# Kernel optimization log

Measured on AMD Instinct MI355X. Metric: run time of the kernel, lower is better.

The kernel has to match this reference:

```python
import jax, jax.numpy as jnp
import numpy as np

NODES, NFEAT = 128, 256


def setup_inputs() -> dict:
    key = jax.random.key(0)
    k1, k2, k3, k4, k5, k6 = jax.random.split(key, 6)
    B = 512
    x = jax.random.normal(k1, (B, NODES, NFEAT), dtype=jnp.float32)
    adj = jax.random.uniform(k2, (B, NODES, NODES), dtype=jnp.float32)
    # GraphConvolution(nfeat, nfeat): weight [nfeat, nfeat], bias [nfeat]
    s = 1.0 / np.sqrt(NFEAT)
    gcn_w = jax.random.uniform(k3, (NFEAT, NFEAT), minval=-s, maxval=s, dtype=jnp.float32)
    gcn_b = jax.random.uniform(k4, (NFEAT,), minval=-s, maxval=s, dtype=jnp.float32)
    # fc: Linear(nfeat*nodes, nfeat), torch layout [out, in]
    s2 = 1.0 / np.sqrt(NFEAT * NODES)
    fc_w = jax.random.uniform(k5, (NFEAT, NFEAT * NODES), minval=-s2, maxval=s2, dtype=jnp.float32)
    fc_b = jax.random.uniform(k6, (NFEAT,), minval=-s2, maxval=s2, dtype=jnp.float32)
    return {"x": x, "adj": adj, "gcn_w": gcn_w, "gcn_b": gcn_b, "fc_w": fc_w, "fc_b": fc_b}


def reference(x, adj, gcn_w, gcn_b, fc_w, fc_b):
    B = x.shape[0]
    # Per-sample loop GCN fused as batched matmuls:
    # support = X @ W ; out = A @ support + b
    support = jnp.einsum('bnf,fg->bng', x, gcn_w)          # [B, nodes, nfeat]
    mid = jnp.einsum('bnm,bmg->bng', adj, support) + gcn_b  # [B, nodes, nfeat]
    # cat along dim0 then reshape(-1, nfeat*nodes) == per-graph flatten
    flat = mid.reshape(B, NODES * NFEAT)
    output = flat @ fc_w.T + fc_b                           # [B, nfeat]
    useful_input = x[:, 0, :]                               # [B, nfeat]
    return (output, useful_input, output)
```

## Files before the change

kernel.cpp:

```cpp
#include <hip/hip_runtime.h>

#define NODES 128
#define NFEAT 256
#define BATCH 512
#define KTOT  (NODES * NFEAT)
#define SPLIT 64
#define KCH   (KTOT / SPLIT)

typedef __bf16 bf16_t;
typedef bf16_t bf16x8 __attribute__((ext_vector_type(8)));
typedef float  f32x4  __attribute__((ext_vector_type(4)));

#define BK   32
#define LDK  40
#define LDM  136
#define TILE 128

__device__ __forceinline__ bf16x8 cvt8(const float4 a, const float4 b) {
    bf16x8 t;
    t[0] = (bf16_t)a.x; t[1] = (bf16_t)a.y; t[2] = (bf16_t)a.z; t[3] = (bf16_t)a.w;
    t[4] = (bf16_t)b.x; t[5] = (bf16_t)b.y; t[6] = (bf16_t)b.z; t[7] = (bf16_t)b.w;
    return t;
}

struct XT { float4 v[4]; };
__device__ __forceinline__ void xload(const float* __restrict__ src, int ld, int k0,
                                      int tid, XT& t) {
#pragma unroll
    for (int i = 0; i < 2; i++) {
        int f = tid + i * 256, r = f >> 2, c = f & 3;
        t.v[2 * i]     = *(const float4*)(src + (size_t)r * ld + k0 + c * 8);
        t.v[2 * i + 1] = *(const float4*)(src + (size_t)r * ld + k0 + c * 8 + 4);
    }
}
__device__ __forceinline__ void xstore(bf16_t* __restrict__ dst, int tid, const XT& t) {
#pragma unroll
    for (int i = 0; i < 2; i++) {
        int f = tid + i * 256, r = f >> 2, c = f & 3;
        *(bf16x8*)(dst + r * LDK + c * 8) = cvt8(t.v[2 * i], t.v[2 * i + 1]);
    }
}

struct AT { bf16x8 v[2]; };
__device__ __forceinline__ void aload(const bf16_t* __restrict__ src, int ld, int k0,
                                      int tid, AT& t) {
#pragma unroll
    for (int i = 0; i < 2; i++) {
        int f = tid + i * 256, r = f >> 2, c = f & 3;
        t.v[i] = *(const bf16x8*)(src + (size_t)r * ld + k0 + c * 8);
    }
}
__device__ __forceinline__ void astore(bf16_t* __restrict__ dst, int tid, const AT& t) {
#pragma unroll
    for (int i = 0; i < 2; i++) {
        int f = tid + i * 256, r = f >> 2, c = f & 3;
        *(bf16x8*)(dst + r * LDK + c * 8) = t.v[i];
    }
}

__global__ __launch_bounds__(256)
void k_wt(const float* __restrict__ w, bf16_t* __restrict__ wT) {
    const int g0 = blockIdx.x * 4;
    const int k  = threadIdx.x;
    const float4 v = *(const float4*)(w + (size_t)k * NFEAT + g0);
    wT[(size_t)(g0 + 0) * NFEAT + k] = (bf16_t)v.x;
    wT[(size_t)(g0 + 1) * NFEAT + k] = (bf16_t)v.y;
    wT[(size_t)(g0 + 2) * NFEAT + k] = (bf16_t)v.z;
    wT[(size_t)(g0 + 3) * NFEAT + k] = (bf16_t)v.w;
}

__global__ __launch_bounds__(256, 3)
void k_fused12(const float* __restrict__ x, const float* __restrict__ adj,
               const bf16_t* __restrict__ wT, const float* __restrict__ gcn_b,
               bf16_t* __restrict__ mid) {
    __shared__ __align__(16) bf16_t As[TILE * LDK];
    __shared__ __align__(16) bf16_t Sb[TILE * LDM];
    const int n0  = blockIdx.x * TILE;
    const int b   = blockIdx.y;
    const int tid = threadIdx.x;
    const int lane = tid & 63, w = tid >> 6, wm = w & 1, wn = w >> 1;
    const int l15 = lane & 15, q = lane >> 4;
    const float* xb   = x   + (size_t)b * NODES * NFEAT;
    const float* adjb = adj + (size_t)b * NODES * NODES;

    const bf16_t* wrow[4];
#pragma unroll
    for (int j = 0; j < 4; j++)
        wrow[j] = wT + (size_t)(n0 + wn * 64 + j * 16 + l15) * NFEAT + q * 8;

    f32x4 acc[4][4] = {};
    {
        XT xt; xload(xb, NFEAT, 0, tid, xt);
        bf16x8 bcur[4], bnxt[4];
#pragma unroll
        for (int j = 0; j < 4; j++) bcur[j] = *(const bf16x8*)(wrow[j]);
        xstore(As, tid, xt);
        __syncthreads();
        for (int k0 = 0; k0 < NFEAT; k0 += BK) {
            const int kn = k0 + BK;
            const bool in = kn < NFEAT;
            XT xn;
            if (in) xload(xb, NFEAT, kn, tid, xn);
            const int knc = in ? kn : 0;
#pragma unroll
            for (int j = 0; j < 4; j++) bnxt[j] = *(const bf16x8*)(wrow[j] + knc);
            bf16x8 a[4];
#pragma unroll
            for (int i = 0; i < 4; i++)
                a[i] = *(const bf16x8*)(As + (wm * 64 + i * 16 + l15) * LDK + q * 8);
#pragma unroll
            for (int i = 0; i < 4; i++)
#pragma unroll
                for (int j = 0; j < 4; j++)
                    acc[i][j] = __builtin_amdgcn_mfma_f32_16x16x32_bf16(a[i], bcur[j], acc[i][j], 0, 0, 0);
            __syncthreads();
            if (in) xstore(As, tid, xn);
#pragma unroll
            for (int j = 0; j < 4; j++) bcur[j] = bnxt[j];
            __syncthreads();
        }
    }

    XT at; xload(adjb, NODES, 0, tid, at);
#pragma unroll
    for (int i = 0; i < 4; i++)
#pragma unroll
        for (int j = 0; j < 4; j++)
#pragma unroll
            for (int r = 0; r < 4; r++) {
                int m = wm * 64 + i * 16 + q * 4 + r;
                int g = wn * 64 + j * 16 + l15;
                Sb[g * LDM + m] = (bf16_t)acc[i][j][r];
            }
    __syncthreads();
    xstore(As, tid, at);
    __syncthreads();

    f32x4 acc2[4][4] = {};
    for (int k0 = 0; k0 < NODES; k0 += BK) {
        const int kn = k0 + BK;
        const bool in = kn < NODES;
        XT xn;
        if (in) xload(adjb, NODES, kn, tid, xn);
        bf16x8 a[4], bb[4];
#pragma unroll
        for (int i = 0; i < 4; i++)
            a[i] = *(const bf16x8*)(As + (wm * 64 + i * 16 + l15) * LDK + q * 8);
#pragma unroll
        for (int j = 0; j < 4; j++)
            bb[j] = *(const bf16x8*)(Sb + (wn * 64 + j * 16 + l15) * LDM + k0 + q * 8);
#pragma unroll
        for (int i = 0; i < 4; i++)
#pragma unroll
            for (int j = 0; j < 4; j++)
                acc2[i][j] = __builtin_amdgcn_mfma_f32_16x16x32_bf16(a[i], bb[j], acc2[i][j], 0, 0, 0);
        __syncthreads();
        if (in) xstore(As, tid, xn);
        __syncthreads();
    }
    bf16_t* outb = mid + (size_t)b * NODES * NFEAT;
#pragma unroll
    for (int j = 0; j < 4; j++) {
        int g = n0 + wn * 64 + j * 16 + l15;
        float bias = gcn_b[g];
#pragma unroll
        for (int i = 0; i < 4; i++)
#pragma unroll
            for (int r = 0; r < 4; r++) {
                int node = wm * 64 + i * 16 + q * 4 + r;
                outb[(size_t)node * NFEAT + g] = (bf16_t)(acc2[i][j][r] + bias);
            }
    }
}

__global__ __launch_bounds__(256, 2)
void k_out(const bf16_t* __restrict__ flat, const float* __restrict__ fcw,
           bf16_t* __restrict__ part) {
    __shared__ __align__(16) bf16_t As[TILE * LDK];
    __shared__ __align__(16) bf16_t Bs[TILE * LDK];
    const int m0 = blockIdx.x * TILE;
    const int n0 = blockIdx.y * TILE;
    const int kb = blockIdx.z * KCH, kend = kb + KCH;
    const int tid = threadIdx.x;
    const int lane = tid & 63, w = tid >> 6, wm = w & 1, wn = w >> 1;
    const int l15 = lane & 15, q = lane >> 4;
    f32x4 acc[4][4] = {};
    const bf16_t* fa = flat + (size_t)m0 * KTOT;
    const float*  fb = fcw + (size_t)n0 * KTOT;

    AT a0; aload(fa, KTOT, kb, tid, a0);
    XT b0; xload(fb, KTOT, kb, tid, b0);
    astore(As, tid, a0);
    xstore(Bs, tid, b0);
    __syncthreads();
    for (int k0 = kb; k0 < kend; k0 += BK) {
        const int kn = k0 + BK;
        const bool in = kn < kend;
        AT an; XT bn;
        if (in) { aload(fa, KTOT, kn, tid, an); xload(fb, KTOT, kn, tid, bn); }
        bf16x8 a[4], bbf[4];
#pragma unroll
        for (int i = 0; i < 4; i++)
            a[i] = *(const bf16x8*)(As + (wm * 64 + i * 16 + l15) * LDK + q * 8);
#pragma unroll
        for (int j = 0; j < 4; j++)
            bbf[j] = *(const bf16x8*)(Bs + (wn * 64 + j * 16 + l15) * LDK + q * 8);
#pragma unroll
        for (int i = 0; i < 4; i++)
#pragma unroll
            for (int j = 0; j < 4; j++)
                acc[i][j] = __builtin_amdgcn_mfma_f32_16x16x32_bf16(a[i], bbf[j], acc[i][j], 0, 0, 0);
        __syncthreads();
        if (in) { astore(As, tid, an); xstore(Bs, tid, bn); }
        __syncthreads();
    }
    bf16_t* pb = part + (size_t)blockIdx.z * BATCH * NFEAT;
#pragma unroll
    for (int i = 0; i < 4; i++)
#pragma unroll
        for (int j = 0; j < 4; j++)
#pragma unroll
            for (int r = 0; r < 4; r++) {
                int bt = m0 + wm * 64 + i * 16 + q * 4 + r;
                int o  = n0 + wn * 64 + j * 16 + l15;
                pb[(size_t)bt * NFEAT + o] = (bf16_t)acc[i][j][r];
            }
}

__global__ __launch_bounds__(256)
void k_reduce(const bf16_t* __restrict__ part, const float* __restrict__ fc_b,
              const float* __restrict__ x, float* __restrict__ out) {
    const int g = blockIdx.x * 256 + threadIdx.x;
    const int o = g & (NFEAT - 1), b = g >> 8;
    float s = fc_b[o];
#pragma unroll
    for (int i = 0; i < SPLIT; i++)
        s += (float)part[(size_t)i * BATCH * NFEAT + g];
    out[g] = s;
    out[BATCH * NFEAT + g] = x[(size_t)b * NODES * NFEAT + o];
    out[2 * BATCH * NFEAT + g] = s;
}

extern "C" void kernel_launch(void* const* d_in, const int* in_sizes, int n_in,
                              void* d_out, int out_size, void* d_ws, size_t ws_size,
                              hipStream_t stream) {
    const float* x     = (const float*)d_in[0];
    const float* adj   = (const float*)d_in[1];
    const float* gcn_w = (const float*)d_in[2];
    const float* gcn_b = (const float*)d_in[3];
    const float* fc_w  = (const float*)d_in[4];
    const float* fc_b  = (const float*)d_in[5];
    float* out = (float*)d_out;

    bf16_t* wT   = (bf16_t*)d_ws;
    bf16_t* mid  = (bf16_t*)((char*)d_ws + 131072);
    bf16_t* part = (bf16_t*)((char*)d_ws + 131072 + (size_t)BATCH * NODES * NFEAT * 2);

    k_wt     <<<dim3(64), dim3(256), 0, stream>>>(gcn_w, wT);
    k_fused12<<<dim3(2, BATCH), dim3(256), 0, stream>>>(x, adj, wT, gcn_b, mid);
    k_out    <<<dim3(4, 2, SPLIT), dim3(256), 0, stream>>>(mid, fc_w, part);
    k_reduce <<<dim3(BATCH), dim3(256), 0, stream>>>(part, fc_b, x, out);
}
```

Before: 209.7 us.

## Replace split-K partial buffer with atomic accumulation, deepen prefetch, widen K tile

New measurement: 238.9 us. 13.9% more time.

```diff
diff --git a/kernel.cpp b/kernel.cpp
--- a/kernel.cpp
+++ b/kernel.cpp
@@ -4,17 +4,19 @@
 #define NFEAT 256
 #define BATCH 512
 #define KTOT  (NODES * NFEAT)
-#define SPLIT 64
+#define SPLIT 128
 #define KCH   (KTOT / SPLIT)
 
 typedef __bf16 bf16_t;
 typedef bf16_t bf16x8 __attribute__((ext_vector_type(8)));
 typedef float  f32x4  __attribute__((ext_vector_type(4)));
 
-#define BK   32
-#define LDK  40
-#define LDM  136
-#define TILE 128
+#define BK    32
+#define LDK   40
+#define BK2   64
+#define LDK2  72
+#define LDM   136
+#define TILE  128
 
 __device__ __forceinline__ bf16x8 cvt8(const float4 a, const float4 b) {
     bf16x8 t;
@@ -41,20 +43,38 @@
     }
 }
 
-struct AT { bf16x8 v[2]; };
-__device__ __forceinline__ void aload(const bf16_t* __restrict__ src, int ld, int k0,
-                                      int tid, AT& t) {
-#pragma unroll
-    for (int i = 0; i < 2; i++) {
-        int f = tid + i * 256, r = f >> 2, c = f & 3;
+struct XT2 { float4 v[8]; };
+__device__ __forceinline__ void xload2(const float* __restrict__ src, int ld, int k0,
+                                       int tid, XT2& t) {
+#pragma unroll
+    for (int i = 0; i < 4; i++) {
+        int f = tid + i * 256, r = f >> 3, c = f & 7;
+        t.v[2 * i]     = *(const float4*)(src + (size_t)r * ld + k0 + c * 8);
+        t.v[2 * i + 1] = *(const float4*)(src + (size_t)r * ld + k0 + c * 8 + 4);
+    }
+}
+__device__ __forceinline__ void xstore2(bf16_t* __restrict__ dst, int tid, const XT2& t) {
+#pragma unroll
+    for (int i = 0; i < 4; i++) {
+        int f = tid + i * 256, r = f >> 3, c = f & 7;
+        *(bf16x8*)(dst + r * LDK2 + c * 8) = cvt8(t.v[2 * i], t.v[2 * i + 1]);
+    }
+}
+
+struct AT2 { bf16x8 v[4]; };
+__device__ __forceinline__ void aload2(const bf16_t* __restrict__ src, int ld, int k0,
+                                       int tid, AT2& t) {
+#pragma unroll
+    for (int i = 0; i < 4; i++) {
+        int f = tid + i * 256, r = f >> 3, c = f & 7;
         t.v[i] = *(const bf16x8*)(src + (size_t)r * ld + k0 + c * 8);
     }
 }
-__device__ __forceinline__ void astore(bf16_t* __restrict__ dst, int tid, const AT& t) {
-#pragma unroll
-    for (int i = 0; i < 2; i++) {
-        int f = tid + i * 256, r = f >> 2, c = f & 3;
-        *(bf16x8*)(dst + r * LDK + c * 8) = t.v[i];
+__device__ __forceinline__ void astore2(bf16_t* __restrict__ dst, int tid, const AT2& t) {
+#pragma unroll
+    for (int i = 0; i < 4; i++) {
+        int f = tid + i * 256, r = f >> 3, c = f & 7;
+        *(bf16x8*)(dst + r * LDK2 + c * 8) = t.v[i];
     }
 }
 
@@ -67,6 +87,21 @@
     wT[(size_t)(g0 + 1) * NFEAT + k] = (bf16_t)v.y;
     wT[(size_t)(g0 + 2) * NFEAT + k] = (bf16_t)v.z;
     wT[(size_t)(g0 + 3) * NFEAT + k] = (bf16_t)v.w;
+}
+
+__global__ __launch_bounds__(256)
+void k_init(const float* __restrict__ fc_b, const float* __restrict__ x,
+            float* __restrict__ out) {
+    const int g = blockIdx.x * 256 + threadIdx.x;
+    const int o = g & (NFEAT - 1), b = g >> 8;
+    out[g] = fc_b[o];
+    out[BATCH * NFEAT + g] = x[(size_t)b * NODES * NFEAT + o];
+}
+
+__global__ __launch_bounds__(256)
+void k_fin(float* __restrict__ out) {
+    const int g = blockIdx.x * 256 + threadIdx.x;
+    out[2 * BATCH * NFEAT + g] = out[g];
 }
 
 __global__ __launch_bounds__(256, 3)
@@ -90,18 +125,19 @@
 
     f32x4 acc[4][4] = {};
     {
-        XT xt; xload(xb, NFEAT, 0, tid, xt);
+        XT r0, rn, r2;
+        xload(xb, NFEAT, 0, tid, r0);
+        xload(xb, NFEAT, BK, tid, rn);
         bf16x8 bcur[4], bnxt[4];
 #pragma unroll
         for (int j = 0; j < 4; j++) bcur[j] = *(const bf16x8*)(wrow[j]);
-        xstore(As, tid, xt);
+        xstore(As, tid, r0);
         __syncthreads();
         for (int k0 = 0; k0 < NFEAT; k0 += BK) {
-            const int kn = k0 + BK;
-            const bool in = kn < NFEAT;
-            XT xn;
-            if (in) xload(xb, NFEAT, kn, tid, xn);
-            const int knc = in ? kn : 0;
+            const bool in1 = (k0 + BK)  < NFEAT;
+            const bool in2 = (k0 + 2*BK) < NFEAT;
+            if (in2) xload(xb, NFEAT, k0 + 2*BK, tid, r2);
+            const int knc = in1 ? k0 + BK : 0;
 #pragma unroll
             for (int j = 0; j < 4; j++) bnxt[j] = *(const bf16x8*)(wrow[j] + knc);
             bf16x8 a[4];
@@ -114,14 +150,17 @@
                 for (int j = 0; j < 4; j++)
                     acc[i][j] = __builtin_amdgcn_mfma_f32_16x16x32_bf16(a[i], bcur[j], acc[i][j], 0, 0, 0);
             __syncthreads();
-            if (in) xstore(As, tid, xn);
+            if (in1) xstore(As, tid, rn);
+            rn = r2;
 #pragma unroll
             for (int j = 0; j < 4; j++) bcur[j] = bnxt[j];
             __syncthreads();
         }
     }
 
-    XT at; xload(adjb, NODES, 0, tid, at);
+    XT a0, a1, a2;
+    xload(adjb, NODES, 0, tid, a0);
+    xload(adjb, NODES, BK, tid, a1);
 #pragma unroll
     for (int i = 0; i < 4; i++)
 #pragma unroll
@@ -133,15 +172,14 @@
                 Sb[g * LDM + m] = (bf16_t)acc[i][j][r];
             }
     __syncthreads();
-    xstore(As, tid, at);
+    xstore(As, tid, a0);
     __syncthreads();
 
     f32x4 acc2[4][4] = {};
     for (int k0 = 0; k0 < NODES; k0 += BK) {
-        const int kn = k0 + BK;
-        const bool in = kn < NODES;
-        XT xn;
-        if (in) xload(adjb, NODES, kn, tid, xn);
+        const bool in1 = (k0 + BK)   < NODES;
+        const bool in2 = (k0 + 2*BK) < NODES;
+        if (in2) xload(adjb, NODES, k0 + 2*BK, tid, a2);
         bf16x8 a[4], bb[4];
 #pragma unroll
         for (int i = 0; i < 4; i++)
@@ -155,7 +193,8 @@
             for (int j = 0; j < 4; j++)
                 acc2[i][j] = __builtin_amdgcn_mfma_f32_16x16x32_bf16(a[i], bb[j], acc2[i][j], 0, 0, 0);
         __syncthreads();
-        if (in) xstore(As, tid, xn);
+        if (in1) xstore(As, tid, a1);
+        a1 = a2;
         __syncthreads();
     }
     bf16_t* outb = mid + (size_t)b * NODES * NFEAT;
@@ -173,11 +212,11 @@
     }
 }
 
-__global__ __launch_bounds__(256, 2)
+__global__ __launch_bounds__(256, 3)
 void k_out(const bf16_t* __restrict__ flat, const float* __restrict__ fcw,
-           bf16_t* __restrict__ part) {
-    __shared__ __align__(16) bf16_t As[TILE * LDK];
-    __shared__ __align__(16) bf16_t Bs[TILE * LDK];
+           float* __restrict__ out) {
+    __shared__ __align__(16) bf16_t As[TILE * LDK2];
+    __shared__ __align__(16) bf16_t Bs[TILE * LDK2];
     const int m0 = blockIdx.x * TILE;
     const int n0 = blockIdx.y * TILE;
     const int kb = blockIdx.z * KCH, kend = kb + KCH;
@@ -188,57 +227,45 @@
     const bf16_t* fa = flat + (size_t)m0 * KTOT;
     const float*  fb = fcw + (size_t)n0 * KTOT;
 
-    AT a0; aload(fa, KTOT, kb, tid, a0);
-    XT b0; xload(fb, KTOT, kb, tid, b0);
-    astore(As, tid, a0);
-    xstore(Bs, tid, b0);
+    AT2 at; aload2(fa, KTOT, kb, tid, at);
+    XT2 bt; xload2(fb, KTOT, kb, tid, bt);
+    astore2(As, tid, at);
+    xstore2(Bs, tid, bt);
     __syncthreads();
-    for (int k0 = kb; k0 < kend; k0 += BK) {
-        const int kn = k0 + BK;
+    for (int k0 = kb; k0 < kend; k0 += BK2) {
+        const int kn = k0 + BK2;
         const bool in = kn < kend;
-        AT an; XT bn;
-        if (in) { aload(fa, KTOT, kn, tid, an); xload(fb, KTOT, kn, tid, bn); }
-        bf16x8 a[4], bbf[4];
-#pragma unroll
-        for (int i = 0; i < 4; i++)
-            a[i] = *(const bf16x8*)(As + (wm * 64 + i * 16 + l15) * LDK + q * 8);
+        AT2 an; XT2 bn;
+        if (in) { aload2(fa, KTOT, kn, tid, an); xload2(fb, KTOT, kn, tid, bn); }
+#pragma unroll
+        for (int kk = 0; kk < BK2; kk += BK) {
+            bf16x8 a[4], bbf[4];
+#pragma unroll
+            for (int i = 0; i < 4; i++)
+                a[i] = *(const bf16x8*)(As + (wm * 64 + i * 16 + l15) * LDK2 + kk + q * 8);
+#pragma unroll
+            for (int j = 0; j < 4; j++)
+                bbf[j] = *(const bf16x8*)(Bs + (wn * 64 + j * 16 + l15) * LDK2 + kk + q * 8);
+#pragma unroll
+            for (int i = 0; i < 4; i++)
+#pragma unroll
+                for (int j = 0; j < 4; j++)
+                    acc[i][j] = __builtin_amdgcn_mfma_f32_16x16x32_bf16(a[i], bbf[j], acc[i][j], 0, 0, 0);
+        }
+        __syncthreads();
+        if (in) { astore2(As, tid, an); xstore2(Bs, tid, bn); }
+        __syncthreads();
+    }
+#pragma unroll
+    for (int i = 0; i < 4; i++)
 #pragma unroll
         for (int j = 0; j < 4; j++)
-            bbf[j] = *(const bf16x8*)(Bs + (wn * 64 + j * 16 + l15) * LDK + q * 8);
-#pragma unroll
-        for (int i = 0; i < 4; i++)
-#pragma unroll
-            for (int j = 0; j < 4; j++)
-                acc[i][j] = __builtin_amdgcn_mfma_f32_16x16x32_bf16(a[i], bbf[j], acc[i][j], 0, 0, 0);
-        __syncthreads();
-        if (in) { astore(As, tid, an); xstore(Bs, tid, bn); }
-        __syncthreads();
-    }
-    bf16_t* pb = part + (size_t)blockIdx.z * BATCH * NFEAT;
-#pragma unroll
-    for (int i = 0; i < 4; i++)
-#pragma unroll
-        for (int j = 0; j < 4; j++)
 #pragma unroll
             for (int r = 0; r < 4; r++) {
-                int bt = m0 + wm * 64 + i * 16 + q * 4 + r;
-                int o  = n0 + wn * 64 + j * 16 + l15;
-                pb[(size_t)bt * NFEAT + o] = (bf16_t)acc[i][j][r];
+                int bt_ = m0 + wm * 64 + i * 16 + q * 4 + r;
+                int o   = n0 + wn * 64 + j * 16 + l15;
+                atomicAdd(&out[(size_t)bt_ * NFEAT + o], acc[i][j][r]);
             }
-}
-
-__global__ __launch_bounds__(256)
-void k_reduce(const bf16_t* __restrict__ part, const float* __restrict__ fc_b,
-              const float* __restrict__ x, float* __restrict__ out) {
-    const int g = blockIdx.x * 256 + threadIdx.x;
-    const int o = g & (NFEAT - 1), b = g >> 8;
-    float s = fc_b[o];
-#pragma unroll
-    for (int i = 0; i < SPLIT; i++)
-        s += (float)part[(size_t)i * BATCH * NFEAT + g];
-    out[g] = s;
-    out[BATCH * NFEAT + g] = x[(size_t)b * NODES * NFEAT + o];
-    out[2 * BATCH * NFEAT + g] = s;
 }
 
 extern "C" void kernel_launch(void* const* d_in, const int* in_sizes, int n_in,
@@ -252,12 +279,12 @@
     const float* fc_b  = (const float*)d_in[5];
     float* out = (float*)d_out;
 
-    bf16_t* wT   = (bf16_t*)d_ws;
-    bf16_t* mid  = (bf16_t*)((char*)d_ws + 131072);
-    bf16_t* part = (bf16_t*)((char*)d_ws + 131072 + (size_t)BATCH * NODES * NFEAT * 2);
+    bf16_t* wT  = (bf16_t*)d_ws;
+    bf16_t* mid = (bf16_t*)((char*)d_ws + 131072);
 
     k_wt     <<<dim3(64), dim3(256), 0, stream>>>(gcn_w, wT);
+    k_init   <<<dim3(BATCH), dim3(256), 0, stream>>>(fc_b, x, out);
     k_fused12<<<dim3(2, BATCH), dim3(256), 0, stream>>>(x, adj, wT, gcn_b, mid);
-    k_out    <<<dim3(4, 2, SPLIT), dim3(256), 0, stream>>>(mid, fc_w, part);
-    k_reduce <<<dim3(BATCH), dim3(256), 0, stream>>>(part, fc_b, x, out);
-}
+    k_out    <<<dim3(4, 2, SPLIT), dim3(256), 0, stream>>>(mid, fc_w, out);
+    k_fin    <<<dim3(BATCH), dim3(256), 0, stream>>>(out);
+}
```
